# Kernel optimization log

Measured on AMD Instinct MI355X. Metric: run time of the kernel, lower is better.

Reference implementation:

```python
import jax, jax.numpy as jnp
import numpy as np

LENGTHSCALE = 0.3
EPS = 1e-10
N = 100000   # evaluation points
M = 3375     # grid_size**3 RBF centers


def setup_inputs() -> dict:
    key = jax.random.key(0)
    k1, k2, k3, k4, k5 = jax.random.split(key, 5)
    x = jax.random.normal(k1, (N, 3), dtype=jnp.float32)
    centers = jax.random.normal(k2, (M, 3), dtype=jnp.float32)
    coeff_u = jax.random.normal(k3, (M,), dtype=jnp.float32)
    coeff_v = jax.random.normal(k4, (M,), dtype=jnp.float32)
    coeff_w = jax.random.normal(k5, (M,), dtype=jnp.float32)
    return {"x": x, "centers": centers, "coeff_u": coeff_u,
            "coeff_v": coeff_v, "coeff_w": coeff_w}


def reference(x, centers, coeff_u, coeff_v, coeff_w):
    # base sphere-attractor field: x * (1 - ||x||)
    r = jnp.linalg.norm(x, axis=-1, keepdims=True)          # (N, 1)
    base = x * (1.0 - r)                                    # (N, 3)

    x_sq = jnp.sum(x * x, axis=-1, keepdims=True)           # (N, 1)
    c_sq = jnp.sum(centers * centers, axis=-1)[None, :]     # (1, M)
    xy = x @ centers.T                                      # (N, M)
    dist2 = jnp.maximum(x_sq + c_sq - 2.0 * xy, EPS)        # (N, M)

    # RBF features and three shared-phi matvecs fused as one matmul
    phi = jnp.exp(-dist2 / (2.0 * LENGTHSCALE ** 2))        # (N, M)
    coeffs = jnp.stack([coeff_u, coeff_v, coeff_w], axis=1) # (M, 3)
    uvw = phi @ coeffs                                      # (N, 3)
    return base + uvw
```

## Files before the change

### kernel.cpp

```cpp
#include <hip/hip_runtime.h>
#include <hip/hip_bf16.h>

#define S2 8.014973f
#define K2 16.029946f
#define CHUNKS 8

typedef float f2 __attribute__((ext_vector_type(2)));

__global__ void rbf_prep_kernel(const float* __restrict__ centers,
                                const float* __restrict__ cu,
                                const float* __restrict__ cv,
                                const float* __restrict__ cw,
                                float4* __restrict__ cpack, int M) {
    int m = blockIdx.x * 256 + threadIdx.x;
    if (m < M) {
        float cx = centers[3 * m + 0];
        float cy = centers[3 * m + 1];
        float cz = centers[3 * m + 2];
        float4 a, b;
        a.x = K2 * cx;
        a.y = K2 * cy;
        a.z = K2 * cz;
        a.w = -S2 * (cx * cx + cy * cy + cz * cz);
        b.x = cu[m];
        b.y = cv[m];
        b.z = cw[m];
        b.w = 0.f;
        cpack[2 * m + 0] = a;
        cpack[2 * m + 1] = b;
    }
}

__global__ __launch_bounds__(512) void rbf_main_kernel(
    const float* __restrict__ x, const float4* __restrict__ cpack,
    float* __restrict__ out, int N, int M) {
    __shared__ float acc[CHUNKS][128][3];

    const int tid = threadIdx.x;
    const int lane = tid & 63;
    const int chunk = __builtin_amdgcn_readfirstlane(tid >> 6);
    const int pbase = blockIdx.x * 128;
    const int p0 = pbase + lane;
    const int p1 = pbase + 64 + lane;

    float x00 = 0.f, x01 = 0.f, x02 = 0.f;
    float x10 = 0.f, x11 = 0.f, x12 = 0.f;
    if (p0 < N) {
        x00 = x[3 * p0 + 0];
        x01 = x[3 * p0 + 1];
        x02 = x[3 * p0 + 2];
    }
    if (p1 < N) {
        x10 = x[3 * p1 + 0];
        x11 = x[3 * p1 + 1];
        x12 = x[3 * p1 + 2];
    }

    const f2 X = {x00, x10};
    const f2 Y = {x01, x11};
    const f2 Z = {x02, x12};
    const f2 PX = {-S2 * (x00 * x00 + x01 * x01 + x02 * x02),
                   -S2 * (x10 * x10 + x11 * x11 + x12 * x12)};

    const int per = (M + CHUNKS - 1) / CHUNKS;
    const int jb = chunk * per;
    const int je = min(jb + per, M);

    f2 au = {0.f, 0.f}, av = {0.f, 0.f}, aw = {0.f, 0.f};

#pragma unroll 4
    for (int j = jb; j < je; ++j) {
        const float4 a = cpack[2 * j + 0];
        const float4 b = cpack[2 * j + 1];
        f2 e = PX + a.w;
        e += Z * a.z;
        e += Y * a.y;
        e += X * a.x;
        f2 phi;
        phi.x = __builtin_amdgcn_exp2f(e.x);
        phi.y = __builtin_amdgcn_exp2f(e.y);
        au += phi * b.x;
        av += phi * b.y;
        aw += phi * b.z;
    }

    if (chunk == 0) {
        float g0 = 1.f - sqrtf(x00 * x00 + x01 * x01 + x02 * x02);
        au.x += x00 * g0;
        av.x += x01 * g0;
        aw.x += x02 * g0;
        float g1 = 1.f - sqrtf(x10 * x10 + x11 * x11 + x12 * x12);
        au.y += x10 * g1;
        av.y += x11 * g1;
        aw.y += x12 * g1;
    }

    acc[chunk][lane][0] = au.x;
    acc[chunk][lane][1] = av.x;
    acc[chunk][lane][2] = aw.x;
    acc[chunk][64 + lane][0] = au.y;
    acc[chunk][64 + lane][1] = av.y;
    acc[chunk][64 + lane][2] = aw.y;
    __syncthreads();

    const int out_n = 3 * N;
    if (tid < 384) {
        int gi = pbase * 3 + tid;
        if (gi < out_n) {
            int pl = tid / 3;
            int c = tid % 3;
            float s = 0.f;
#pragma unroll
            for (int k = 0; k < CHUNKS; ++k) s += acc[k][pl][c];
            out[gi] = s;
        }
    }
}

extern "C" void kernel_launch(void* const* d_in, const int* in_sizes, int n_in,
                              void* d_out, int out_size, void* d_ws,
                              size_t ws_size, hipStream_t stream) {
    const float* x = (const float*)d_in[0];
    const float* centers = (const float*)d_in[1];
    const float* cu = (const float*)d_in[2];
    const float* cv = (const float*)d_in[3];
    const float* cw = (const float*)d_in[4];
    const int N = in_sizes[0] / 3;
    const int M = in_sizes[1] / 3;
    float4* cpack = (float4*)d_ws;
    float* out = (float*)d_out;

    hipLaunchKernelGGL(rbf_prep_kernel, dim3((M + 255) / 256), dim3(256), 0,
                       stream, centers, cu, cv, cw, cpack, M);
    hipLaunchKernelGGL(rbf_main_kernel, dim3((N + 127) / 128), dim3(512), 0,
                       stream, x, cpack, out, N, M);
}
```

Before: 139.5 us.

## Use persistent per-wave tile×chunk tasks with atomic accumulation into output

Replaces the fixed 8-way split of centers inside each 512-thread block with a persistent grid of 2048 blocks of 4 waves. Each wave loops over (point-tile, center-chunk) tasks, splitting the centers into 21 chunks, and adds its partial sums straight into the output with global float atomics after a memset. This drops the shared-memory reduction and __syncthreads and is meant to balance work across the CUs. The cost is an extra memset, many atomic adds to global memory, reloading x once per chunk, and a summation order that is no longer deterministic.

```diff
diff --git a/kernel.cpp b/kernel.cpp
--- a/kernel.cpp
+++ b/kernel.cpp
@@ -3,7 +3,7 @@
 
 #define S2 8.014973f
 #define K2 16.029946f
-#define CHUNKS 8
+#define NCHUNK 21
 
 typedef float f2 __attribute__((ext_vector_type(2)));
 
@@ -31,88 +31,81 @@
     }
 }
 
-__global__ __launch_bounds__(512) void rbf_main_kernel(
+__global__ __launch_bounds__(256) void rbf_main_kernel(
     const float* __restrict__ x, const float4* __restrict__ cpack,
-    float* __restrict__ out, int N, int M) {
-    __shared__ float acc[CHUNKS][128][3];
-
+    float* __restrict__ out, int N, int M, int NT, int per, int ntask) {
     const int tid = threadIdx.x;
     const int lane = tid & 63;
-    const int chunk = __builtin_amdgcn_readfirstlane(tid >> 6);
-    const int pbase = blockIdx.x * 128;
-    const int p0 = pbase + lane;
-    const int p1 = pbase + 64 + lane;
+    const int wave0 =
+        __builtin_amdgcn_readfirstlane(blockIdx.x * 4 + (tid >> 6));
+    const int nwaves = gridDim.x * 4;
 
-    float x00 = 0.f, x01 = 0.f, x02 = 0.f;
-    float x10 = 0.f, x11 = 0.f, x12 = 0.f;
-    if (p0 < N) {
-        x00 = x[3 * p0 + 0];
-        x01 = x[3 * p0 + 1];
-        x02 = x[3 * p0 + 2];
-    }
-    if (p1 < N) {
-        x10 = x[3 * p1 + 0];
-        x11 = x[3 * p1 + 1];
-        x12 = x[3 * p1 + 2];
-    }
+    for (int task = wave0; task < ntask; task += nwaves) {
+        const int tile = task % NT;
+        const int chunk = task / NT;
+        const int p0 = tile * 128 + lane;
+        const int p1 = p0 + 64;
 
-    const f2 X = {x00, x10};
-    const f2 Y = {x01, x11};
-    const f2 Z = {x02, x12};
-    const f2 PX = {-S2 * (x00 * x00 + x01 * x01 + x02 * x02),
-                   -S2 * (x10 * x10 + x11 * x11 + x12 * x12)};
+        float x00 = 0.f, x01 = 0.f, x02 = 0.f;
+        float x10 = 0.f, x11 = 0.f, x12 = 0.f;
+        if (p0 < N) {
+            x00 = x[3 * p0 + 0];
+            x01 = x[3 * p0 + 1];
+            x02 = x[3 * p0 + 2];
+        }
+        if (p1 < N) {
+            x10 = x[3 * p1 + 0];
+            x11 = x[3 * p1 + 1];
+            x12 = x[3 * p1 + 2];
+        }
 
-    const int per = (M + CHUNKS - 1) / CHUNKS;
-    const int jb = chunk * per;
-    const int je = min(jb + per, M);
+        const f2 X = {x00, x10};
+        const f2 Y = {x01, x11};
+        const f2 Z = {x02, x12};
+        const f2 PX = {-S2 * (x00 * x00 + x01 * x01 + x02 * x02),
+                       -S2 * (x10 * x10 + x11 * x11 + x12 * x12)};
 
-    f2 au = {0.f, 0.f}, av = {0.f, 0.f}, aw = {0.f, 0.f};
+        const int jb = chunk * per;
+        const int je = min(jb + per, M);
+
+        f2 au = {0.f, 0.f}, av = {0.f, 0.f}, aw = {0.f, 0.f};
 
 #pragma unroll 4
-    for (int j = jb; j < je; ++j) {
-        const float4 a = cpack[2 * j + 0];
-        const float4 b = cpack[2 * j + 1];
-        f2 e = PX + a.w;
-        e += Z * a.z;
-        e += Y * a.y;
-        e += X * a.x;
-        f2 phi;
-        phi.x = __builtin_amdgcn_exp2f(e.x);
-        phi.y = __builtin_amdgcn_exp2f(e.y);
-        au += phi * b.x;
-        av += phi * b.y;
-        aw += phi * b.z;
-    }
+        for (int j = jb; j < je; ++j) {
+            const float4 a = cpack[2 * j + 0];
+            const float4 b = cpack[2 * j + 1];
+            f2 e = PX + a.w;
+            e += Z * a.z;
+            e += Y * a.y;
+            e += X * a.x;
+            f2 phi;
+            phi.x = __builtin_amdgcn_exp2f(e.x);
+            phi.y = __builtin_amdgcn_exp2f(e.y);
+            au += phi * b.x;
+            av += phi * b.y;
+            aw += phi * b.z;
+        }
 
-    if (chunk == 0) {
-        float g0 = 1.f - sqrtf(x00 * x00 + x01 * x01 + x02 * x02);
-        au.x += x00 * g0;
-        av.x += x01 * g0;
-        aw.x += x02 * g0;
-        float g1 = 1.f - sqrtf(x10 * x10 + x11 * x11 + x12 * x12);
-        au.y += x10 * g1;
-        av.y += x11 * g1;
-        aw.y += x12 * g1;
-    }
+        if (chunk == 0) {
+            float g0 = 1.f - sqrtf(x00 * x00 + x01 * x01 + x02 * x02);
+            au.x += x00 * g0;
+            av.x += x01 * g0;
+            aw.x += x02 * g0;
+            float g1 = 1.f - sqrtf(x10 * x10 + x11 * x11 + x12 * x12);
+            au.y += x10 * g1;
+            av.y += x11 * g1;
+            aw.y += x12 * g1;
+        }
 
-    acc[chunk][lane][0] = au.x;
-    acc[chunk][lane][1] = av.x;
-    acc[chunk][lane][2] = aw.x;
-    acc[chunk][64 + lane][0] = au.y;
-    acc[chunk][64 + lane][1] = av.y;
-    acc[chunk][64 + lane][2] = aw.y;
-    __syncthreads();
-
-    const int out_n = 3 * N;
-    if (tid < 384) {
-        int gi = pbase * 3 + tid;
-        if (gi < out_n) {
-            int pl = tid / 3;
-            int c = tid % 3;
-            float s = 0.f;
-#pragma unroll
-            for (int k = 0; k < CHUNKS; ++k) s += acc[k][pl][c];
-            out[gi] = s;
+        if (p0 < N) {
+            atomicAdd(&out[3 * p0 + 0], au.x);
+            atomicAdd(&out[3 * p0 + 1], av.x);
+            atomicAdd(&out[3 * p0 + 2], aw.x);
+        }
+        if (p1 < N) {
+            atomicAdd(&out[3 * p1 + 0], au.y);
+            atomicAdd(&out[3 * p1 + 1], av.y);
+            atomicAdd(&out[3 * p1 + 2], aw.y);
         }
     }
 }
@@ -130,8 +123,13 @@
     float4* cpack = (float4*)d_ws;
     float* out = (float*)d_out;
 
+    const int NT = (N + 127) / 128;
+    const int per = (M + NCHUNK - 1) / NCHUNK;
+    const int ntask = NT * NCHUNK;
+
     hipLaunchKernelGGL(rbf_prep_kernel, dim3((M + 255) / 256), dim3(256), 0,
                        stream, centers, cu, cv, cw, cpack, M);
-    hipLaunchKernelGGL(rbf_main_kernel, dim3((N + 127) / 128), dim3(512), 0,
-                       stream, x, cpack, out, N, M);
+    hipMemsetAsync(d_out, 0, (size_t)out_size * sizeof(float), stream);
+    hipLaunchKernelGGL(rbf_main_kernel, dim3(2048), dim3(256), 0, stream, x,
+                       cpack, out, N, M, NT, per, ntask);
 }
```

Result: slower. 146.8 us (+5.2%).
